# Optimization experiments

Hardware: AMD Instinct MI355X
Metric: run time of the kernel (lower is better)

## Reference

```python
import jax, jax.numpy as jnp
import numpy as np

WIN_LEN = 400
HOP = 100
NFFT = 512


def _make_kernel():
    # rfft of identity -> DFT basis, truncated to window length
    fb = np.fft.rfft(np.eye(NFFT))[:WIN_LEN]          # [WIN_LEN, NFFT//2+1] complex
    kernel = np.concatenate([fb.real, fb.imag], axis=1).T  # [2*(NFFT//2+1), WIN_LEN]
    # periodic (fftbins=True) Hamming window, as scipy.signal.get_window('hamming', N, fftbins=True)
    n = np.arange(WIN_LEN)
    window = (0.54 - 0.46 * np.cos(2.0 * np.pi * n / WIN_LEN)).astype(np.float32)
    kernel = kernel.astype(np.float32)[:, None, :] * window  # [514, 1, WIN_LEN]
    return jnp.asarray(kernel)


def setup_inputs() -> dict:
    key = jax.random.key(0)
    x = jax.random.normal(key, (32, 480000), dtype=jnp.float32)  # [B, T] raw audio
    return {"x": x, "weight": _make_kernel()}


def reference(x, weight):
    # x: [B, T] -> [B, 1, T]; pad both sides by (window_len - hop)
    pad = WIN_LEN - HOP
    xp = jnp.pad(x[:, None, :], ((0, 0), (0, 0), (pad, pad)))
    # strided conv against fixed Fourier basis -> [B, 2*(NFFT//2+1), n_frames]
    out = jax.lax.conv_general_dilated(
        xp, weight,
        window_strides=(HOP,),
        padding='VALID',
        dimension_numbers=('NCH', 'OIH', 'NCH'),
    )
    return out
```

## Files before the change

### kernel.cpp

```cpp
#include <hip/hip_runtime.h>
#include <hip/hip_bf16.h>


#define T_LEN   480000
#define NF      4803
#define C_OUT   514
#define HOP     100
#define WIN     400
#define BM      128
#define BN      64
#define WSTR    424
#define XPS     487040
#define XP_TOTAL (32 * XPS)
#define WP_ROWS 576
#define WP_ELEMS (WP_ROWS * WSTR)
#define WP_BYTE_OFF ((size_t)XP_TOTAL * 2)
#define WS_NEEDED (WP_BYTE_OFF + (size_t)WP_ELEMS * 2)
#define MT_CNT  38
#define NT_CNT  9
#define NTILES  (NT_CNT * MT_CNT * 32)
#define TPNT    (MT_CNT * 32)
#define XSEG    13312

typedef __attribute__((ext_vector_type(8))) short short8;
typedef __attribute__((ext_vector_type(4))) float f32x4;

__device__ __forceinline__ unsigned short f2bf(float f) {
    unsigned int u = __float_as_uint(f);
    u += 0x7FFFu + ((u >> 16) & 1u);
    return (unsigned short)(u >> 16);
}

__device__ __forceinline__ void gl_lds16(const unsigned short* g, unsigned short* l) {
    __builtin_amdgcn_global_load_lds(
        (const __attribute__((address_space(1))) unsigned int*)(g),
        (__attribute__((address_space(3))) unsigned int*)(l), 16, 0, 0);
}

__global__ void cvt_x_kernel(const float* __restrict__ x, unsigned short* __restrict__ xp) {
    const int t = blockIdx.x * 256 + threadIdx.x;
    const int b  = t / (XPS / 4);
    const int i4 = t - b * (XPS / 4);
    const int i  = i4 * 4;
    const int g  = i - 300;
    ushort4 h;
    if (g >= 0 && g + 3 < T_LEN) {
        const float4 f = *(const float4*)(x + (size_t)b * T_LEN + g);
        h.x = f2bf(f.x); h.y = f2bf(f.y); h.z = f2bf(f.z); h.w = f2bf(f.w);
    } else {
        const float* xb = x + (size_t)b * T_LEN;
        h.x = (g + 0 >= 0 && g + 0 < T_LEN) ? f2bf(xb[g + 0]) : 0;
        h.y = (g + 1 >= 0 && g + 1 < T_LEN) ? f2bf(xb[g + 1]) : 0;
        h.z = (g + 2 >= 0 && g + 2 < T_LEN) ? f2bf(xb[g + 2]) : 0;
        h.w = (g + 3 >= 0 && g + 3 < T_LEN) ? f2bf(xb[g + 3]) : 0;
    }
    *(ushort4*)(xp + (size_t)b * XPS + i) = h;
}

__global__ void cvt_w_kernel(const float* __restrict__ w, unsigned short* __restrict__ wp) {
    const int t = blockIdx.x * 256 + threadIdx.x;
    if (t >= WP_ELEMS) return;
    const int c = t / WSTR;
    const int k = t - c * WSTR;
    wp[t] = (c < C_OUT && k < WIN) ? f2bf(w[(size_t)c * WIN + k]) : 0;
}

__device__ __forceinline__ void decode_tile(int t, int& nt, int& b, int& mt) {
    nt = t / TPNT;
    const int rem = t - nt * TPNT;
    b  = rem / MT_CNT;
    mt = rem - b * MT_CNT;
}

__global__ __launch_bounds__(512, 1)
void stft_gemm(const unsigned short* __restrict__ xp,
               const unsigned short* __restrict__ wp,
               float* __restrict__ out) {
    __shared__ unsigned short w_s[BN * WSTR];
    __shared__ unsigned short x_s[2][XSEG];

    const int tid  = threadIdx.x;
    const int lane = tid & 63;
    const int wv   = tid >> 6;

    const int id = blockIdx.x;
    const int t0 = (id < 192) ? id * 43 : 192 * 43 + (id - 192) * 42;
    const int nti = (id < 192) ? 43 : 42;

    int nt, b, mt;
    decode_tile(t0, nt, b, mt);

    {
        const unsigned short* wg = wp + (size_t)nt * (BN * WSTR);
        #pragma unroll
        for (int c = wv; c < 53; c += 8) {
            const int idx = (c << 6) + lane;
            gl_lds16(wg + idx * 8, w_s + idx * 8);
        }
        const unsigned short* xg = xp + (size_t)b * XPS + mt * (BM * HOP);
        #pragma unroll
        for (int c = wv; c < 26; c += 8) {
            const int idx = (c << 6) + lane;
            gl_lds16(xg + idx * 8, x_s[0] + idx * 8);
        }
    }
    __syncthreads();

    const int q4 = lane >> 4;
    const int lm = lane & 15;
    const int wr = wv & 3;
    const int wc = wv >> 2;

    int aoff[2];
    #pragma unroll
    for (int mi = 0; mi < 2; ++mi) aoff[mi] = (wr * 32 + mi * 16 + lm) * HOP + q4 * 8;
    int boff[2];
    #pragma unroll
    for (int ni = 0; ni < 2; ++ni) boff[ni] = (wc * 32 + ni * 16 + lm) * WSTR + q4 * 8;

    int cur = 0;
    for (int ti = 0; ti < nti; ++ti) {
        int nnt = nt, nb = 0, nmt = 0;
        const bool have_next = (ti + 1 < nti);
        if (have_next) {
            decode_tile(t0 + ti + 1, nnt, nb, nmt);
            const unsigned short* xg = xp + (size_t)nb * XPS + nmt * (BM * HOP);
            unsigned short* xd = x_s[cur ^ 1];
            #pragma unroll
            for (int c = wv; c < 26; c += 8) {
                const int idx = (c << 6) + lane;
                gl_lds16(xg + idx * 8, xd + idx * 8);
            }
        }

        const unsigned short* xs = x_s[cur];
        f32x4 acc[2][2];
        #pragma unroll
        for (int mi = 0; mi < 2; ++mi)
            #pragma unroll
            for (int ni = 0; ni < 2; ++ni)
                acc[mi][ni] = (f32x4){0.f, 0.f, 0.f, 0.f};

        #pragma unroll
        for (int kc = 0; kc < 13; ++kc) {
            const int k = kc * 32;
            union { short8 v; unsigned long long u[2]; } au[2];
            #pragma unroll
            for (int mi = 0; mi < 2; ++mi) {
                const unsigned long long* p = (const unsigned long long*)(xs + aoff[mi] + k);
                au[mi].u[0] = p[0]; au[mi].u[1] = p[1];
            }
            #pragma unroll
            for (int ni = 0; ni < 2; ++ni) {
                const short8 bf = *(const short8*)(&w_s[boff[ni] + k]);
                #pragma unroll
                for (int mi = 0; mi < 2; ++mi)
                    acc[mi][ni] = __builtin_amdgcn_mfma_f32_16x16x32_bf16(au[mi].v, bf, acc[mi][ni], 0, 0, 0);
            }
        }

        float* ob = out + (size_t)b * C_OUT * NF;
        const int f_base = mt * BM + wr * 32 + q4 * 4;
        const int c_base = nt * BN + wc * 32 + lm;
        #pragma unroll
        for (int mi = 0; mi < 2; ++mi) {
            const int fg = f_base + mi * 16;
            const bool fok = (fg + 3 < NF);
            #pragma unroll
            for (int ni = 0; ni < 2; ++ni) {
                const int cg = c_base + ni * 16;
                if (cg < C_OUT) {
                    float* op = ob + (size_t)cg * NF + fg;
                    if (fok) {
                        op[0] = acc[mi][ni][0]; op[1] = acc[mi][ni][1];
                        op[2] = acc[mi][ni][2]; op[3] = acc[mi][ni][3];
                    } else {
                        #pragma unroll
                        for (int r = 0; r < 4; ++r)
                            if (fg + r < NF) op[r] = acc[mi][ni][r];
                    }
                }
            }
        }

        __syncthreads();
        if (have_next && nnt != nt) {
            const unsigned short* wg = wp + (size_t)nnt * (BN * WSTR);
            #pragma unroll
            for (int c = wv; c < 53; c += 8) {
                const int idx = (c << 6) + lane;
                gl_lds16(wg + idx * 8, w_s + idx * 8);
            }
            __syncthreads();
        }
        nt = nnt; b = nb; mt = nmt;
        cur ^= 1;
    }
}

#define SEG 13120
__global__ __launch_bounds__(256, 2)
void conv_stft_fallback(const float* __restrict__ x,
                        const float* __restrict__ w,
                        float* __restrict__ out) {
    __shared__ short x_s[SEG];
    __shared__ short w_s[BN * WSTR];
    const int tid = threadIdx.x;
    const int nt  = blockIdx.x;
    const int mt  = blockIdx.y;
    const int b   = blockIdx.z;
    const int s0 = mt * (BM * HOP) - 300;
    const float* xb = x + (size_t)b * T_LEN;
    for (int v = tid; v < SEG / 4; v += 256) {
        int g = s0 + v * 4;
        float f0, f1, f2, f3;
        if (g >= 0 && g + 3 < T_LEN) {
            const float4 f = *(const float4*)(xb + g);
            f0 = f.x; f1 = f.y; f2 = f.z; f3 = f.w;
        } else {
            f0 = (g + 0 >= 0 && g + 0 < T_LEN) ? xb[g + 0] : 0.f;
            f1 = (g + 1 >= 0 && g + 1 < T_LEN) ? xb[g + 1] : 0.f;
            f2 = (g + 2 >= 0 && g + 2 < T_LEN) ? xb[g + 2] : 0.f;
            f3 = (g + 3 >= 0 && g + 3 < T_LEN) ? xb[g + 3] : 0.f;
        }
        ushort4 h; h.x = f2bf(f0); h.y = f2bf(f1); h.z = f2bf(f2); h.w = f2bf(f3);
        *(ushort4*)(&x_s[v * 4]) = h;
    }
    for (int s = tid; s < BN * 106; s += 256) {
        const int r  = s / 106;
        const int gk = s - r * 106;
        const int c  = nt * BN + r;
        ushort4 h = make_ushort4(0, 0, 0, 0);
        if (gk < 100 && c < C_OUT) {
            const float4 f = *(const float4*)(w + (size_t)c * WIN + gk * 4);
            h.x = f2bf(f.x); h.y = f2bf(f.y); h.z = f2bf(f.z); h.w = f2bf(f.w);
        }
        if (gk * 4 < WSTR) *(ushort4*)(&w_s[r * WSTR + gk * 4]) = h;
    }
    __syncthreads();
    const int lane = tid & 63, wv = tid >> 6, q = lane >> 4, lm = lane & 15;
    f32x4 acc[2][4];
    #pragma unroll
    for (int mi = 0; mi < 2; ++mi)
        #pragma unroll
        for (int ni = 0; ni < 4; ++ni) acc[mi][ni] = (f32x4){0.f,0.f,0.f,0.f};
    const int a0 = (wv * 32 + lm) * HOP + q * 8;
    const int a1 = a0 + 16 * HOP;
    int boff[4];
    #pragma unroll
    for (int ni = 0; ni < 4; ++ni) boff[ni] = (ni * 16 + lm) * WSTR + q * 8;
    #pragma unroll
    for (int kc = 0; kc < 13; ++kc) {
        const int k = kc * 32;
        union { short8 v; unsigned long long u[2]; } au0, au1;
        const unsigned long long* p0 = (const unsigned long long*)(x_s + a0 + k);
        const unsigned long long* p1 = (const unsigned long long*)(x_s + a1 + k);
        au0.u[0] = p0[0]; au0.u[1] = p0[1];
        au1.u[0] = p1[0]; au1.u[1] = p1[1];
        #pragma unroll
        for (int ni = 0; ni < 4; ++ni) {
            const short8 bf = *(const short8*)(&w_s[boff[ni] + k]);
            acc[0][ni] = __builtin_amdgcn_mfma_f32_16x16x32_bf16(au0.v, bf, acc[0][ni], 0, 0, 0);
            acc[1][ni] = __builtin_amdgcn_mfma_f32_16x16x32_bf16(au1.v, bf, acc[1][ni], 0, 0, 0);
        }
    }
    float* ob = out + (size_t)b * C_OUT * NF;
    const int f_base = mt * BM + wv * 32 + q * 4;
    const int c_base = nt * BN + lm;
    #pragma unroll
    for (int mi = 0; mi < 2; ++mi) {
        #pragma unroll
        for (int ni = 0; ni < 4; ++ni) {
            const int cg = c_base + ni * 16;
            if (cg < C_OUT) {
                float* op = ob + (size_t)cg * NF;
                #pragma unroll
                for (int r = 0; r < 4; ++r) {
                    const int fg = f_base + mi * 16 + r;
                    if (fg < NF) op[fg] = acc[mi][ni][r];
                }
            }
        }
    }
}

extern "C" void kernel_launch(void* const* d_in, const int* in_sizes, int n_in,
                              void* d_out, int out_size, void* d_ws, size_t ws_size,
                              hipStream_t stream) {
    const float* x = (const float*)d_in[0];
    const float* w = (const float*)d_in[1];
    float* out = (float*)d_out;

    if (ws_size >= WS_NEEDED) {
        unsigned short* xp = (unsigned short*)d_ws;
        unsigned short* wp = (unsigned short*)((char*)d_ws + WP_BYTE_OFF);
        cvt_x_kernel<<<XP_TOTAL / 4 / 256, 256, 0, stream>>>(x, xp);
        cvt_w_kernel<<<(WP_ELEMS + 255) / 256, 256, 0, stream>>>(w, wp);
        stft_gemm<<<dim3(256), 512, 0, stream>>>(xp, wp, out);
    } else {
        dim3 grid(NT_CNT, MT_CNT, 32);
        conv_stft_fallback<<<grid, 256, 0, stream>>>(x, w, out);
    }
}
```

Baseline: 467.5 us.

## Fuse bf16 conversion into persistent STFT GEMM and use nontemporal output stores

Drops the separate x and weight bf16 conversion kernels and the workspace staging. The persistent GEMM now reads fp32 audio into registers for the next tile, converts it after the MFMA loop and writes it to LDS, and converts weights when staging them into LDS. This removes an extra full pass over the input plus two kernel launches. In exchange, each tile's x segment is read as fp32 (twice the bytes of bf16) and converted redundantly across the 9 N-tiles, and register pressure rises. Output stores become nontemporal vector stores.

```diff
diff --git a/kernel.cpp b/kernel.cpp
--- a/kernel.cpp
+++ b/kernel.cpp
@@ -1,5 +1,4 @@
 #include <hip/hip_runtime.h>
-#include <hip/hip_bf16.h>
 
 
 #define T_LEN   480000
@@ -10,17 +9,13 @@
 #define BM      128
 #define BN      64
 #define WSTR    424
-#define XPS     487040
-#define XP_TOTAL (32 * XPS)
-#define WP_ROWS 576
-#define WP_ELEMS (WP_ROWS * WSTR)
-#define WP_BYTE_OFF ((size_t)XP_TOTAL * 2)
-#define WS_NEEDED (WP_BYTE_OFF + (size_t)WP_ELEMS * 2)
 #define MT_CNT  38
 #define NT_CNT  9
 #define NTILES  (NT_CNT * MT_CNT * 32)
 #define TPNT    (MT_CNT * 32)
 #define XSEG    13312
+#define NCHUNK  3280
+#define XLOC    7
 
 typedef __attribute__((ext_vector_type(8))) short short8;
 typedef __attribute__((ext_vector_type(4))) float f32x4;
@@ -29,40 +24,6 @@
     unsigned int u = __float_as_uint(f);
     u += 0x7FFFu + ((u >> 16) & 1u);
     return (unsigned short)(u >> 16);
-}
-
-__device__ __forceinline__ void gl_lds16(const unsigned short* g, unsigned short* l) {
-    __builtin_amdgcn_global_load_lds(
-        (const __attribute__((address_space(1))) unsigned int*)(g),
-        (__attribute__((address_space(3))) unsigned int*)(l), 16, 0, 0);
-}
-
-__global__ void cvt_x_kernel(const float* __restrict__ x, unsigned short* __restrict__ xp) {
-    const int t = blockIdx.x * 256 + threadIdx.x;
-    const int b  = t / (XPS / 4);
-    const int i4 = t - b * (XPS / 4);
-    const int i  = i4 * 4;
-    const int g  = i - 300;
-    ushort4 h;
-    if (g >= 0 && g + 3 < T_LEN) {
-        const float4 f = *(const float4*)(x + (size_t)b * T_LEN + g);
-        h.x = f2bf(f.x); h.y = f2bf(f.y); h.z = f2bf(f.z); h.w = f2bf(f.w);
-    } else {
-        const float* xb = x + (size_t)b * T_LEN;
-        h.x = (g + 0 >= 0 && g + 0 < T_LEN) ? f2bf(xb[g + 0]) : 0;
-        h.y = (g + 1 >= 0 && g + 1 < T_LEN) ? f2bf(xb[g + 1]) : 0;
-        h.z = (g + 2 >= 0 && g + 2 < T_LEN) ? f2bf(xb[g + 2]) : 0;
-        h.w = (g + 3 >= 0 && g + 3 < T_LEN) ? f2bf(xb[g + 3]) : 0;
-    }
-    *(ushort4*)(xp + (size_t)b * XPS + i) = h;
-}
-
-__global__ void cvt_w_kernel(const float* __restrict__ w, unsigned short* __restrict__ wp) {
-    const int t = blockIdx.x * 256 + threadIdx.x;
-    if (t >= WP_ELEMS) return;
-    const int c = t / WSTR;
-    const int k = t - c * WSTR;
-    wp[t] = (c < C_OUT && k < WIN) ? f2bf(w[(size_t)c * WIN + k]) : 0;
 }
 
 __device__ __forceinline__ void decode_tile(int t, int& nt, int& b, int& mt) {
@@ -72,10 +33,42 @@
     mt = rem - b * MT_CNT;
 }
 
+__device__ __forceinline__ void stage_w(const float* __restrict__ w,
+                                        unsigned short* __restrict__ w_s,
+                                        int nt, int tid) {
+    for (int lin = tid; lin < BN * (WSTR / 4); lin += 512) {
+        const int r  = lin / (WSTR / 4);
+        const int j  = lin - r * (WSTR / 4);
+        const int k0 = j * 4;
+        const int c  = nt * BN + r;
+        ushort4 h = make_ushort4(0, 0, 0, 0);
+        if (c < C_OUT && k0 < WIN) {
+            const float4 f = *(const float4*)(w + (size_t)c * WIN + k0);
+            h.x = f2bf(f.x); h.y = f2bf(f.y); h.z = f2bf(f.z); h.w = f2bf(f.w);
+        }
+        *(ushort4*)(w_s + r * WSTR + k0) = h;
+    }
+}
+
+__device__ __forceinline__ float4 load_chunk(const float* __restrict__ xb,
+                                             int base, int c) {
+    const int g = base + c * 4;
+    float4 f;
+    if (g >= 0 && g <= T_LEN - 4) {
+        f = *(const float4*)(xb + g);
+    } else {
+        f.x = (g + 0 >= 0 && g + 0 < T_LEN) ? xb[g + 0] : 0.f;
+        f.y = (g + 1 >= 0 && g + 1 < T_LEN) ? xb[g + 1] : 0.f;
+        f.z = (g + 2 >= 0 && g + 2 < T_LEN) ? xb[g + 2] : 0.f;
+        f.w = (g + 3 >= 0 && g + 3 < T_LEN) ? xb[g + 3] : 0.f;
+    }
+    return f;
+}
+
 __global__ __launch_bounds__(512, 1)
-void stft_gemm(const unsigned short* __restrict__ xp,
-               const unsigned short* __restrict__ wp,
-               float* __restrict__ out) {
+void stft_fused(const float* __restrict__ x,
+                const float* __restrict__ w,
+                float* __restrict__ out) {
     __shared__ unsigned short w_s[BN * WSTR];
     __shared__ unsigned short x_s[2][XSEG];
 
@@ -83,25 +76,26 @@
     const int lane = tid & 63;
     const int wv   = tid >> 6;
 
-    const int id = blockIdx.x;
-    const int t0 = (id < 192) ? id * 43 : 192 * 43 + (id - 192) * 42;
+    const int id  = blockIdx.x;
+    const int t0  = (id < 192) ? id * 43 : 192 * 43 + (id - 192) * 42;
     const int nti = (id < 192) ? 43 : 42;
 
     int nt, b, mt;
     decode_tile(t0, nt, b, mt);
 
+    stage_w(w, w_s, nt, tid);
     {
-        const unsigned short* wg = wp + (size_t)nt * (BN * WSTR);
-        #pragma unroll
-        for (int c = wv; c < 53; c += 8) {
-            const int idx = (c << 6) + lane;
-            gl_lds16(wg + idx * 8, w_s + idx * 8);
-        }
-        const unsigned short* xg = xp + (size_t)b * XPS + mt * (BM * HOP);
-        #pragma unroll
-        for (int c = wv; c < 26; c += 8) {
-            const int idx = (c << 6) + lane;
-            gl_lds16(xg + idx * 8, x_s[0] + idx * 8);
+        const float* xb = x + (size_t)b * T_LEN;
+        const int base = mt * (BM * HOP) - 300;
+        #pragma unroll
+        for (int j = 0; j < XLOC; ++j) {
+            const int c = tid + j * 512;
+            if (c < NCHUNK) {
+                const float4 f = load_chunk(xb, base, c);
+                ushort4 h;
+                h.x = f2bf(f.x); h.y = f2bf(f.y); h.z = f2bf(f.z); h.w = f2bf(f.w);
+                *(ushort4*)(x_s[0] + c * 4) = h;
+            }
         }
     }
     __syncthreads();
@@ -122,14 +116,21 @@
     for (int ti = 0; ti < nti; ++ti) {
         int nnt = nt, nb = 0, nmt = 0;
         const bool have_next = (ti + 1 < nti);
+        float4 r0, r1, r2, r3, r4, r5, r6;
         if (have_next) {
             decode_tile(t0 + ti + 1, nnt, nb, nmt);
-            const unsigned short* xg = xp + (size_t)nb * XPS + nmt * (BM * HOP);
-            unsigned short* xd = x_s[cur ^ 1];
-            #pragma unroll
-            for (int c = wv; c < 26; c += 8) {
-                const int idx = (c << 6) + lane;
-                gl_lds16(xg + idx * 8, xd + idx * 8);
+            const float* xb = x + (size_t)nb * T_LEN;
+            const int base = nmt * (BM * HOP) - 300;
+            r0 = load_chunk(xb, base, tid + 0 * 512);
+            r1 = load_chunk(xb, base, tid + 1 * 512);
+            r2 = load_chunk(xb, base, tid + 2 * 512);
+            r3 = load_chunk(xb, base, tid + 3 * 512);
+            r4 = load_chunk(xb, base, tid + 4 * 512);
+            r5 = load_chunk(xb, base, tid + 5 * 512);
+            if (tid + 6 * 512 < NCHUNK) {
+                r6 = load_chunk(xb, base, tid + 6 * 512);
+            } else {
+                r6 = (float4){0.f, 0.f, 0.f, 0.f};
             }
         }
 
@@ -159,6 +160,21 @@
             }
         }
 
+        if (have_next) {
+            unsigned short* xd = x_s[cur ^ 1];
+            const float4 rr[XLOC] = {r0, r1, r2, r3, r4, r5, r6};
+            #pragma unroll
+            for (int j = 0; j < XLOC; ++j) {
+                const int c = tid + j * 512;
+                if (c < NCHUNK) {
+                    ushort4 h;
+                    h.x = f2bf(rr[j].x); h.y = f2bf(rr[j].y);
+                    h.z = f2bf(rr[j].z); h.w = f2bf(rr[j].w);
+                    *(ushort4*)(xd + c * 4) = h;
+                }
+            }
+        }
+
         float* ob = out + (size_t)b * C_OUT * NF;
         const int f_base = mt * BM + wr * 32 + q4 * 4;
         const int c_base = nt * BN + wc * 32 + lm;
@@ -172,12 +188,11 @@
                 if (cg < C_OUT) {
                     float* op = ob + (size_t)cg * NF + fg;
                     if (fok) {
-                        op[0] = acc[mi][ni][0]; op[1] = acc[mi][ni][1];
-                        op[2] = acc[mi][ni][2]; op[3] = acc[mi][ni][3];
+                        __builtin_nontemporal_store(acc[mi][ni], (f32x4*)op);
                     } else {
                         #pragma unroll
-                        for (int r = 0; r < 4; ++r)
-                            if (fg + r < NF) op[r] = acc[mi][ni][r];
+                        for (int rI = 0; rI < 4; ++rI)
+                            if (fg + rI < NF) __builtin_nontemporal_store(acc[mi][ni][rI], op + rI);
                     }
                 }
             }
@@ -185,102 +200,11 @@
 
         __syncthreads();
         if (have_next && nnt != nt) {
-            const unsigned short* wg = wp + (size_t)nnt * (BN * WSTR);
-            #pragma unroll
-            for (int c = wv; c < 53; c += 8) {
-                const int idx = (c << 6) + lane;
-                gl_lds16(wg + idx * 8, w_s + idx * 8);
-            }
+            stage_w(w, w_s, nnt, tid);
             __syncthreads();
         }
         nt = nnt; b = nb; mt = nmt;
         cur ^= 1;
-    }
-}
-
-#define SEG 13120
-__global__ __launch_bounds__(256, 2)
-void conv_stft_fallback(const float* __restrict__ x,
-                        const float* __restrict__ w,
-                        float* __restrict__ out) {
-    __shared__ short x_s[SEG];
-    __shared__ short w_s[BN * WSTR];
-    const int tid = threadIdx.x;
-    const int nt  = blockIdx.x;
-    const int mt  = blockIdx.y;
-    const int b   = blockIdx.z;
-    const int s0 = mt * (BM * HOP) - 300;
-    const float* xb = x + (size_t)b * T_LEN;
-    for (int v = tid; v < SEG / 4; v += 256) {
-        int g = s0 + v * 4;
-        float f0, f1, f2, f3;
-        if (g >= 0 && g + 3 < T_LEN) {
-            const float4 f = *(const float4*)(xb + g);
-            f0 = f.x; f1 = f.y; f2 = f.z; f3 = f.w;
-        } else {
-            f0 = (g + 0 >= 0 && g + 0 < T_LEN) ? xb[g + 0] : 0.f;
-            f1 = (g + 1 >= 0 && g + 1 < T_LEN) ? xb[g + 1] : 0.f;
-            f2 = (g + 2 >= 0 && g + 2 < T_LEN) ? xb[g + 2] : 0.f;
-            f3 = (g + 3 >= 0 && g + 3 < T_LEN) ? xb[g + 3] : 0.f;
-        }
-        ushort4 h; h.x = f2bf(f0); h.y = f2bf(f1); h.z = f2bf(f2); h.w = f2bf(f3);
-        *(ushort4*)(&x_s[v * 4]) = h;
-    }
-    for (int s = tid; s < BN * 106; s += 256) {
-        const int r  = s / 106;
-        const int gk = s - r * 106;
-        const int c  = nt * BN + r;
-        ushort4 h = make_ushort4(0, 0, 0, 0);
-        if (gk < 100 && c < C_OUT) {
-            const float4 f = *(const float4*)(w + (size_t)c * WIN + gk * 4);
-            h.x = f2bf(f.x); h.y = f2bf(f.y); h.z = f2bf(f.z); h.w = f2bf(f.w);
-        }
-        if (gk * 4 < WSTR) *(ushort4*)(&w_s[r * WSTR + gk * 4]) = h;
-    }
-    __syncthreads();
-    const int lane = tid & 63, wv = tid >> 6, q = lane >> 4, lm = lane & 15;
-    f32x4 acc[2][4];
-    #pragma unroll
-    for (int mi = 0; mi < 2; ++mi)
-        #pragma unroll
-        for (int ni = 0; ni < 4; ++ni) acc[mi][ni] = (f32x4){0.f,0.f,0.f,0.f};
-    const int a0 = (wv * 32 + lm) * HOP + q * 8;
-    const int a1 = a0 + 16 * HOP;
-    int boff[4];
-    #pragma unroll
-    for (int ni = 0; ni < 4; ++ni) boff[ni] = (ni * 16 + lm) * WSTR + q * 8;
-    #pragma unroll
-    for (int kc = 0; kc < 13; ++kc) {
-        const int k = kc * 32;
-        union { short8 v; unsigned long long u[2]; } au0, au1;
-        const unsigned long long* p0 = (const unsigned long long*)(x_s + a0 + k);
-        const unsigned long long* p1 = (const unsigned long long*)(x_s + a1 + k);
-        au0.u[0] = p0[0]; au0.u[1] = p0[1];
-        au1.u[0] = p1[0]; au1.u[1] = p1[1];
-        #pragma unroll
-        for (int ni = 0; ni < 4; ++ni) {
-            const short8 bf = *(const short8*)(&w_s[boff[ni] + k]);
-            acc[0][ni] = __builtin_amdgcn_mfma_f32_16x16x32_bf16(au0.v, bf, acc[0][ni], 0, 0, 0);
-            acc[1][ni] = __builtin_amdgcn_mfma_f32_16x16x32_bf16(au1.v, bf, acc[1][ni], 0, 0, 0);
-        }
-    }
-    float* ob = out + (size_t)b * C_OUT * NF;
-    const int f_base = mt * BM + wv * 32 + q * 4;
-    const int c_base = nt * BN + lm;
-    #pragma unroll
-    for (int mi = 0; mi < 2; ++mi) {
-        #pragma unroll
-        for (int ni = 0; ni < 4; ++ni) {
-            const int cg = c_base + ni * 16;
-            if (cg < C_OUT) {
-                float* op = ob + (size_t)cg * NF;
-                #pragma unroll
-                for (int r = 0; r < 4; ++r) {
-                    const int fg = f_base + mi * 16 + r;
-                    if (fg < NF) op[fg] = acc[mi][ni][r];
-                }
-            }
-        }
     }
 }
 
@@ -290,15 +214,7 @@
     const float* x = (const float*)d_in[0];
     const float* w = (const float*)d_in[1];
     float* out = (float*)d_out;
-
-    if (ws_size >= WS_NEEDED) {
-        unsigned short* xp = (unsigned short*)d_ws;
-        unsigned short* wp = (unsigned short*)((char*)d_ws + WP_BYTE_OFF);
-        cvt_x_kernel<<<XP_TOTAL / 4 / 256, 256, 0, stream>>>(x, xp);
-        cvt_w_kernel<<<(WP_ELEMS + 255) / 256, 256, 0, stream>>>(w, wp);
-        stft_gemm<<<dim3(256), 512, 0, stream>>>(xp, wp, out);
-    } else {
-        dim3 grid(NT_CNT, MT_CNT, 32);
-        conv_stft_fallback<<<grid, 256, 0, stream>>>(x, w, out);
-    }
-}
+    (void)d_ws; (void)ws_size;
+
+    stft_fused<<<dim3(256), 512, 0, stream>>>(x, w, out);
+}
```

Result: slower. 621.9 us (+33.0%).
